# Kernel tuning notes

Measured on AMD Instinct MI355X. Metric: run time of the kernel, lower is better.

Reference implementation:

```python
import jax, jax.numpy as jnp
import numpy as np

B, L, D = 4, 4096, 1024  # batch, seq, d_model == in_features == out_features
E, R = 8, 8              # n_experts, r_base
DH = D // 2              # router hidden


def setup_inputs() -> dict:
    key = jax.random.key(0)
    ks = jax.random.split(key, 8)
    s = 0.02
    return {
        "x": jax.random.normal(ks[0], (B, L, D), dtype=jnp.float32),
        "W_base": jax.random.normal(ks[1], (D, D), dtype=jnp.float32) * s,
        "router_W1": jax.random.normal(ks[2], (DH, D), dtype=jnp.float32) * s,
        "router_b1": jnp.zeros((DH,), dtype=jnp.float32),
        "router_W2": jax.random.normal(ks[3], (E, DH), dtype=jnp.float32) * s,
        "router_b2": jnp.zeros((E,), dtype=jnp.float32),
        "temperature": jnp.asarray(1.0, dtype=jnp.float32),
        "lora_A": jax.random.normal(ks[4], (E, R, D), dtype=jnp.float32) * s,
        "lora_B": jax.random.normal(ks[5], (E, D, R), dtype=jnp.float32) * s,
    }


def reference(x, W_base, router_W1, router_b1, router_W2, router_b2,
              temperature, lora_A, lora_B):
    # Base frozen linear (bias=False): [B,L,D]
    base = jnp.einsum("bld,od->blo", x, W_base)
    # Router (eval mode: dropout inactive). hidden_states = x (Identity projection).
    h = jax.nn.relu(jnp.einsum("bld,hd->blh", x, router_W1) + router_b1)
    logits = (jnp.einsum("blh,eh->ble", h, router_W2) + router_b2) / temperature
    gates = jax.nn.softmax(logits, axis=-1)  # softmax over experts, [B,L,E]
    # All experts' low-rank projections batched: x @ A_e.T -> [B,L,E,R]
    xa = jnp.einsum("bld,erd->bler", x, lora_A)
    # Gate-weighted up-projection and sum over experts: [B,L,D]
    lora_out = jnp.einsum("bler,ble,edr->bld", xa, gates, lora_B)
    return base + lora_out
```

## Files before the change

### kernel.cpp

```cpp
#include <hip/hip_runtime.h>
#include <hip/hip_bf16.h>
#include <stdint.h>
#include <math.h>


#define M_TOK 16384

typedef unsigned short u16;
typedef short bf16x8 __attribute__((ext_vector_type(8)));
typedef float f32x4 __attribute__((ext_vector_type(4)));
typedef __attribute__((address_space(3))) uint32_t lds_u32_t;
typedef __attribute__((address_space(1))) const uint32_t glb_u32_t;

__device__ __forceinline__ u16 f2bf(float f) {
  uint32_t u = __builtin_bit_cast(uint32_t, f);
  return (u16)((u + 0x7fffu + ((u >> 16) & 1u)) >> 16);
}
__device__ __forceinline__ int cvtpk(float lo, float hi) {
  int r;
  asm("v_cvt_pk_bf16_f32 %0, %1, %2" : "=v"(r) : "v"(lo), "v"(hi));
  return r;
}

#define VMCNT(n) asm volatile("s_waitcnt vmcnt(%0)" ::"i"(n) : "memory")
#define LGKM0 asm volatile("s_waitcnt lgkmcnt(0)" ::: "memory")
#define BAR asm volatile("s_barrier" ::: "memory")
#define MEMFENCE asm volatile("" ::: "memory")
#define SP(x) __builtin_amdgcn_s_setprio(x)

__global__ __launch_bounds__(256) void prep_k(const float* __restrict__ Wb,
                                              const float* __restrict__ rW1,
                                              const float* __restrict__ rW2,
                                              const float* __restrict__ loraA,
                                              const float* __restrict__ loraB,
                                              u16* __restrict__ Btb,
                                              u16* __restrict__ W1b,
                                              u16* __restrict__ W2b,
                                              u16* __restrict__ A2b) {
  const int g = blockIdx.x;
  const int tid = threadIdx.x;
  if (g < 1024) {
    int i = g * 256 + tid;
    int idx = i * 4;
    int row = idx >> 10, col = idx & 1023;
    float4 v = ((const float4*)Wb)[i];
    ushort4 o;
    o.x = f2bf(v.x); o.y = f2bf(v.y); o.z = f2bf(v.z); o.w = f2bf(v.w);
    *(ushort4*)(Btb + (size_t)row * 1088 + col) = o;
  } else if (g < 1536) {
    int i = (g - 1024) * 256 + tid;
    float4 v = ((const float4*)rW1)[i];
    ushort4 o;
    o.x = f2bf(v.x); o.y = f2bf(v.y); o.z = f2bf(v.z); o.w = f2bf(v.w);
    ((ushort4*)W1b)[i] = o;
  } else if (g < 1792) {
    int idx = (g - 1536) * 256 + tid;
    int n = idx >> 6, q = idx & 63;
    int e = q >> 3, r = q & 7;
    Btb[(size_t)n * 1088 + 1024 + q] = f2bf(loraB[((size_t)(e * 1024 + n)) * 8 + r]);
  } else if (g < 1856) {
    int i = (g - 1792) * 256 + tid;
    float4 v = ((const float4*)loraA)[i];
    ushort4 o;
    o.x = f2bf(v.x); o.y = f2bf(v.y); o.z = f2bf(v.z); o.w = f2bf(v.w);
    ((ushort4*)A2b)[i] = o;
  } else {
    int i = (g - 1856) * 256 + tid;
    int idx = i * 4;
    int row = idx >> 9, col = idx & 511;
    ushort4 o = {0, 0, 0, 0};
    if (row < 8) {
      float4 v = *(const float4*)(rW2 + (size_t)row * 512 + col);
      o.x = f2bf(v.x); o.y = f2bf(v.y); o.z = f2bf(v.z); o.w = f2bf(v.w);
    }
    ((ushort4*)W2b)[i] = o;
  }
}

__global__ __launch_bounds__(512, 2) void gemm_h(const float* __restrict__ x,
                                                 const u16* __restrict__ W1b,
                                                 const u16* __restrict__ W2bv,
                                                 const u16* __restrict__ A2bv,
                                                 u16* __restrict__ xb,
                                                 u16* __restrict__ wb,
                                                 const float* __restrict__ b1,
                                                 const float* __restrict__ b2,
                                                 const float* __restrict__ temp,
                                                 const int K) {
  constexpr int ABUF = 64 * 128;
  constexpr int BBUF = 512 * 128;
  constexpr int A2BUF = 64 * 128;
  constexpr int BUFB = ABUF + BBUF + A2BUF;
  __shared__ __align__(16) uint8_t lds[2 * BUFB];

  const int tid = threadIdx.x;
  const int lane = tid & 63, w = tid >> 6;
  const int l15 = lane & 15, lhi = lane >> 4;
  const int xorv = (lane & 7) << 4;
  const int c0 = (lhi * 16) ^ xorv;
  const int c1 = (64 + lhi * 16) ^ xorv;

  const int f = blockIdx.x;
  const int m0 = ((f & 7) * 32 + (f >> 3)) * 64;

  const int nk = K >> 6;
  const int rot = (f >> 3) & (nk - 1);
  auto PH = [&](int l) { int lc = l < nk ? l : nk - 1; return (lc + rot) & (nk - 1); };

  const int xrow = tid >> 3, xsub = tid & 7;

  f32x4 acc[4][4] = {};
  f32x4 wacc[4] = {};
  bf16x8 af[4][2], bfv[4][2], a2f[2];
  float4 xA0, xA1, xB0, xB1;

  auto stageBH = [&](int ktp, int b) {
    uint8_t* dst = lds + b * BUFB + ABUF + w * 1024;
#pragma unroll
    for (int i = 0; i < 8; ++i) {
      const int off = i * 8192 + tid * 16;
      const int row = off >> 7;
      const int ss = ((off >> 4) & 7) ^ (row & 7);
      const uint8_t* g =
          (const uint8_t*)W1b + (size_t)row * 2048 + ktp * 128 + ss * 16;
      __builtin_amdgcn_global_load_lds((glb_u32_t*)g, (lds_u32_t*)(dst + i * 8192),
                                       16, 0, 0);
    }
  };
  auto stageA2 = [&](int ktp, int b) {
    uint8_t* dst = lds + b * BUFB + ABUF + BBUF + w * 1024;
    const int off = tid * 16;
    const int row = off >> 7;
    const int ss = ((off >> 4) & 7) ^ (row & 7);
    const uint8_t* g =
        (const uint8_t*)A2bv + (size_t)row * 2048 + ktp * 128 + ss * 16;
    __builtin_amdgcn_global_load_lds((glb_u32_t*)g, (lds_u32_t*)dst, 16, 0, 0);
  };
  auto issueX = [&](int ktp, float4& ra, float4& rb) {
    const float* gp = x + (size_t)(m0 + xrow) * 1024 + ktp * 64 + xsub * 8;
    ra = *(const float4*)gp;
    rb = *(const float4*)(gp + 4);
  };
  auto writeA = [&](int ktp, int b, const float4& ra, const float4& rb) {
    int4 sv;
    sv.x = cvtpk(ra.x, ra.y); sv.y = cvtpk(ra.z, ra.w);
    sv.z = cvtpk(rb.x, rb.y); sv.w = cvtpk(rb.z, rb.w);
    *(int4*)(lds + b * BUFB + xrow * 128 + ((xsub ^ (xrow & 7)) << 4)) = sv;
    *(int4*)(xb + (size_t)(m0 + xrow) * 1024 + ktp * 64 + xsub * 8) = sv;
  };
  auto loadAH = [&](const uint8_t* bufA) {
#pragma unroll
    for (int mf = 0; mf < 4; ++mf) {
      const uint8_t* pr = bufA + (mf * 16 + l15) * 128;
      af[mf][0] = *(const bf16x8*)(pr + c0);
      af[mf][1] = *(const bf16x8*)(pr + c1);
    }
  };
  auto loadBH = [&](const uint8_t* bufB) {
#pragma unroll
    for (int nf = 0; nf < 4; ++nf) {
      const uint8_t* pr = bufB + (w * 64 + nf * 16 + l15) * 128;
      bfv[nf][0] = *(const bf16x8*)(pr + c0);
      bfv[nf][1] = *(const bf16x8*)(pr + c1);
    }
  };
  auto loadA2 = [&](const uint8_t* base) {
    const uint8_t* pr = base + ABUF + BBUF + ((w & 3) * 16 + l15) * 128;
    a2f[0] = *(const bf16x8*)(pr + c0);
    a2f[1] = *(const bf16x8*)(pr + c1);
  };

#define HMM()                                                                  \
  _Pragma("unroll") for (int mf = 0; mf < 4; ++mf)                             \
  _Pragma("unroll") for (int nf = 0; nf < 4; ++nf)                             \
  _Pragma("unroll") for (int ks = 0; ks < 2; ++ks)                             \
      acc[mf][nf] = __builtin_amdgcn_mfma_f32_16x16x32_bf16(                   \
          af[mf][ks], bfv[nf][ks], acc[mf][nf], 0, 0, 0);
#define WMM()                                                                  \
  _Pragma("unroll") for (int mf = 0; mf < 4; ++mf)                             \
  _Pragma("unroll") for (int ks = 0; ks < 2; ++ks)                             \
      wacc[mf] = __builtin_amdgcn_mfma_f32_16x16x32_bf16(                      \
          af[mf][ks], a2f[ks], wacc[mf], 0, 0, 0);

  {
    const float* gp = x + (size_t)(m0 + xrow) * 1024 + rot * 64 + xsub * 8;
    float4 a = *(const float4*)gp, b = *(const float4*)(gp + 4);
    int4 sv;
    sv.x = cvtpk(a.x, a.y); sv.y = cvtpk(a.z, a.w);
    sv.z = cvtpk(b.x, b.y); sv.w = cvtpk(b.z, b.w);
    *(int4*)(lds + xrow * 128 + ((xsub ^ (xrow & 7)) << 4)) = sv;
    *(int4*)(xb + (size_t)(m0 + xrow) * 1024 + rot * 64 + xsub * 8) = sv;
  }
  stageBH(rot, 0);
  stageA2(rot, 0);
  MEMFENCE;
  issueX(PH(1), xA0, xA1);
  VMCNT(2);
  LGKM0;
  BAR;

  const int nit = nk >> 1;
#pragma unroll 1
  for (int it = 0; it < nit; ++it) {
    const int t = it * 2;
    stageBH(PH(t + 1), 1);
    stageA2(PH(t + 1), 1);
    MEMFENCE;
    loadAH(lds);
    loadBH(lds + ABUF);
    loadA2(lds);
    issueX(PH(t + 2), xB0, xB1);
    MEMFENCE;
    VMCNT(11);
    writeA(PH(t + 1), 1, xA0, xA1);
    SP(1); HMM(); WMM(); SP(0);
    LGKM0; VMCNT(3); BAR;
    stageBH(PH(t + 2), 0);
    stageA2(PH(t + 2), 0);
    MEMFENCE;
    loadAH(lds + BUFB);
    loadBH(lds + BUFB + ABUF);
    loadA2(lds + BUFB);
    issueX(PH(t + 3), xA0, xA1);
    MEMFENCE;
    VMCNT(11);
    writeA(PH(t + 2), 0, xB0, xB1);
    SP(1); HMM(); WMM(); SP(0);
    LGKM0; VMCNT(3); BAR;
  }

  u16* hs = (u16*)lds;
  float* g_lds = (float*)(lds + 66560);
  __syncthreads();
#pragma unroll
  for (int mf = 0; mf < 4; ++mf) {
#pragma unroll
    for (int nf = 0; nf < 4; ++nf) {
      const int col = w * 64 + nf * 16 + l15;
#pragma unroll
      for (int j = 0; j < 4; ++j) {
        const int row = mf * 16 + lhi * 4 + j;
        float v = fmaxf(acc[mf][nf][j] + b1[col], 0.f);
        hs[row * 520 + col] = f2bf(v);
      }
    }
  }
  __syncthreads();
  if (w < 4) {
    f32x4 acc2 = {};
#pragma unroll
    for (int ks = 0; ks < 16; ++ks) {
      bf16x8 bfrag = *(const bf16x8*)(W2bv + (size_t)l15 * 512 + ks * 32 + lhi * 8);
      bf16x8 afrag = *(const bf16x8*)(hs + (w * 16 + l15) * 520 + ks * 32 + lhi * 8);
      acc2 = __builtin_amdgcn_mfma_f32_16x16x32_bf16(afrag, bfrag, acc2, 0, 0, 0);
    }
    if (l15 < 8) {
      float t = temp[0];
      float lg[4];
#pragma unroll
      for (int j = 0; j < 4; ++j) lg[j] = (acc2[j] + b2[l15]) / t;
      float mx[4], sm[4];
#pragma unroll
      for (int j = 0; j < 4; ++j) mx[j] = lg[j];
#pragma unroll
      for (int m = 1; m <= 4; m <<= 1)
#pragma unroll
        for (int j = 0; j < 4; ++j) mx[j] = fmaxf(mx[j], __shfl_xor(mx[j], m));
#pragma unroll
      for (int j = 0; j < 4; ++j) { lg[j] = expf(lg[j] - mx[j]); sm[j] = lg[j]; }
#pragma unroll
      for (int m = 1; m <= 4; m <<= 1)
#pragma unroll
        for (int j = 0; j < 4; ++j) sm[j] += __shfl_xor(sm[j], m);
#pragma unroll
      for (int j = 0; j < 4; ++j)
        g_lds[(w * 16 + lhi * 4 + j) * 8 + l15] = lg[j] / sm[j];
    }
  }
  __syncthreads();
  if (w < 4) {
#pragma unroll
    for (int mf = 0; mf < 4; ++mf) {
#pragma unroll
      for (int j = 0; j < 4; ++j) {
        const int row = mf * 16 + lhi * 4 + j;
        const int col = w * 16 + l15;
        float v = wacc[mf][j] * g_lds[row * 8 + (col >> 3)];
        wb[(size_t)(m0 + row) * 64 + col] = f2bf(v);
      }
    }
  }
}

#define MFMA_Q2(mh, nh, AF, BF)                                                \
  _Pragma("unroll") for (int im2 = 0; im2 < 4; ++im2)                          \
  _Pragma("unroll") for (int in2 = 0; in2 < 2; ++in2)                          \
  _Pragma("unroll") for (int ks = 0; ks < 2; ++ks)                             \
      acc[(mh) * 4 + im2][(nh) * 2 + in2] =                                    \
          __builtin_amdgcn_mfma_f32_16x16x32_bf16(                             \
              AF[im2][ks], BF[in2][ks],                                        \
              acc[(mh) * 4 + im2][(nh) * 2 + in2], 0, 0, 0);

__global__ __launch_bounds__(512, 2) void gemm_out(const u16* __restrict__ A,
                                                   const u16* __restrict__ Bt,
                                                   const u16* __restrict__ A2,
                                                   float* __restrict__ C,
                                                   const int N, const int K,
                                                   const int lda, const int ldb) {
  constexpr int BM = 256, BN = 256;
  constexpr int VMC = 4;
  constexpr int BUFB = (BM + BN) * 128;

  __shared__ __align__(16) uint8_t lds[2 * BUFB];

  const int tid = threadIdx.x;
  const int lane = tid & 63, w = tid >> 6;
  const int wr = w >> 2, wcn = w & 3;
  const int l15 = lane & 15, lhi = lane >> 4;
  const int xorv = (lane & 7) << 4;
  const int c0 = (lhi * 16) ^ xorv;
  const int c1 = (64 + lhi * 16) ^ xorv;

  const int f = blockIdx.x;
  const int idx = (f & 7) * 32 + (f >> 3);
  const int gx = N / BN;
  const int m0 = (idx / gx) * BM;
  const int n0 = (idx % gx) * BN;

  const size_t lda_b = (size_t)lda * 2, ldb_b = (size_t)ldb * 2;
  const int nk = K >> 6;
  const int arow0 = (wr * (BM / 2) + l15) * 128;
  const int brow0 = (wcn * (BN / 4) + l15) * 128;

  f32x4 acc[8][4] = {};
  bf16x8 A0f[4][2], A1f[4][2];
  bf16x8 B0f[2][2], B1f[2][2];

  auto stageA = [&](int h, int kt, int b) {
    const int ktc = kt < nk ? kt : nk - 1;
    const bool last = (ktc == nk - 1);
    uint8_t* dst = lds + b * BUFB + h * (BM * 64) + w * 1024;
#pragma unroll
    for (int i = 0; i < 2; ++i) {
      const int off = i * 8192 + tid * 16;
      const int row = h * (BM / 2) + (off >> 7);
      const int ss = ((off >> 4) & 7) ^ (row & 7);
      const uint8_t* g =
          last ? (const uint8_t*)A2 + (size_t)(m0 + row) * 128 + ss * 16
               : (const uint8_t*)A + (size_t)(m0 + row) * lda_b + ktc * 128 + ss * 16;
      __builtin_amdgcn_global_load_lds((glb_u32_t*)g, (lds_u32_t*)(dst + i * 8192),
                                       16, 0, 0);
    }
  };
  auto stageB = [&](int h, int kt, int b) {
    const int ktc = kt < nk ? kt : nk - 1;
    uint8_t* dst = lds + b * BUFB + BM * 128 + h * (BN * 64) + w * 1024;
#pragma unroll
    for (int i = 0; i < 2; ++i) {
      const int off = i * 8192 + tid * 16;
      const int row = h * (BN / 2) + (off >> 7);
      const int ss = ((off >> 4) & 7) ^ (row & 7);
      const uint8_t* g =
          (const uint8_t*)Bt + (size_t)(n0 + row) * ldb_b + ktc * 128 + ss * 16;
      __builtin_amdgcn_global_load_lds((glb_u32_t*)g, (lds_u32_t*)(dst + i * 8192),
                                       16, 0, 0);
    }
  };
  auto loadA = [&](int mh, const uint8_t* buf, bf16x8 (&dst)[4][2]) {
#pragma unroll
    for (int im2 = 0; im2 < 4; ++im2) {
      const uint8_t* p = buf + arow0 + mh * (4 * 2048) + im2 * 2048;
      dst[im2][0] = *(const bf16x8*)(p + c0);
      dst[im2][1] = *(const bf16x8*)(p + c1);
    }
  };
  auto loadB = [&](int nh, const uint8_t* buf, bf16x8 (&dst)[2][2]) {
#pragma unroll
    for (int in2 = 0; in2 < 2; ++in2) {
      const uint8_t* p = buf + BM * 128 + brow0 + nh * (2 * 2048) + in2 * 2048;
      dst[in2][0] = *(const bf16x8*)(p + c0);
      dst[in2][1] = *(const bf16x8*)(p + c1);
    }
  };

  const uint8_t* b0 = lds;
  const uint8_t* b1 = lds + BUFB;

  stageA(0, 0, 0); stageA(1, 0, 0);
  stageB(0, 0, 0); stageB(1, 0, 0);
  stageB(0, 1, 1); stageB(1, 1, 1);
  VMCNT(VMC); BAR;
  loadA(0, b0, A0f); loadB(0, b0, B0f);

  const int NIT = nk >> 1;
#pragma unroll 1
  for (int it = 0; it < NIT; ++it) {
    const int t = it * 2;
    stageA(0, t + 1, 1);
    BAR;
    SP(1); MFMA_Q2(0, 0, A0f, B0f); SP(0);
    loadB(1, b0, B1f);
    BAR;
    stageA(1, t + 1, 1);
    BAR;
    SP(1); MFMA_Q2(0, 1, A0f, B1f); SP(0);
    loadA(1, b0, A1f);
    BAR;
    stageB(0, t + 2, 0);
    BAR;
    SP(1); MFMA_Q2(1, 1, A1f, B1f); SP(0);
    BAR;
    stageB(1, t + 2, 0);
    VMCNT(VMC);
    BAR;
    SP(1); MFMA_Q2(1, 0, A1f, B0f); SP(0);
    loadA(0, b1, A0f); loadB(0, b1, B0f);
    BAR;
    stageA(0, t + 2, 0);
    BAR;
    SP(1); MFMA_Q2(0, 0, A0f, B0f); SP(0);
    loadB(1, b1, B1f);
    BAR;
    stageA(1, t + 2, 0);
    BAR;
    SP(1); MFMA_Q2(0, 1, A0f, B1f); SP(0);
    loadA(1, b1, A1f);
    BAR;
    stageB(0, t + 3, 1);
    BAR;
    SP(1); MFMA_Q2(1, 1, A1f, B1f); SP(0);
    BAR;
    stageB(1, t + 3, 1);
    VMCNT(VMC);
    BAR;
    SP(1); MFMA_Q2(1, 0, A1f, B0f); SP(0);
    loadA(0, b0, A0f); loadB(0, b0, B0f);
    BAR;
  }

  if (nk & 1) {
    SP(1); MFMA_Q2(0, 0, A0f, B0f); SP(0);
    loadB(1, b0, B1f);
    SP(1); MFMA_Q2(0, 1, A0f, B1f); SP(0);
    loadA(1, b0, A1f);
    SP(1); MFMA_Q2(1, 1, A1f, B1f); MFMA_Q2(1, 0, A1f, B0f); SP(0);
  }

#pragma unroll
  for (int im = 0; im < 8; ++im) {
#pragma unroll
    for (int in_ = 0; in_ < 4; ++in_) {
      const int col = n0 + wcn * 64 + in_ * 16 + l15;
#pragma unroll
      for (int j = 0; j < 4; ++j) {
        const int row = m0 + wr * 128 + im * 16 + lhi * 4 + j;
        C[(size_t)row * N + col] = acc[im][in_][j];
      }
    }
  }
}

extern "C" void kernel_launch(void* const* d_in, const int* in_sizes, int n_in,
                              void* d_out, int out_size, void* d_ws, size_t ws_size,
                              hipStream_t stream) {
  const float* x     = (const float*)d_in[0];
  const float* Wb    = (const float*)d_in[1];
  const float* rW1   = (const float*)d_in[2];
  const float* rb1   = (const float*)d_in[3];
  const float* rW2   = (const float*)d_in[4];
  const float* rb2   = (const float*)d_in[5];
  const float* temp  = (const float*)d_in[6];
  const float* loraA = (const float*)d_in[7];
  const float* loraB = (const float*)d_in[8];
  float* out = (float*)d_out;

  uint8_t* p = (uint8_t*)d_ws;
  u16* xb    = (u16*)p;   p += (size_t)M_TOK * 1024 * 2;
  u16* wb    = (u16*)p;   p += (size_t)M_TOK * 64 * 2;
  u16* Btb   = (u16*)p;   p += (size_t)1024 * 1088 * 2;
  u16* W1b   = (u16*)p;   p += (size_t)512 * 1024 * 2;
  u16* W2b   = (u16*)p;   p += (size_t)16 * 512 * 2;
  u16* A2b   = (u16*)p;   p += (size_t)64 * 1024 * 2;

  prep_k<<<1864, 256, 0, stream>>>(Wb, rW1, rW2, loraA, loraB, Btb, W1b, W2b, A2b);

  gemm_h<<<256, 512, 0, stream>>>(x, W1b, W2b, A2b, xb, wb, rb1, rb2, temp, 1024);

  gemm_out<<<256, 512, 0, stream>>>(xb, Btb, wb, out, 1024, 1088, 1024, 1088);
}
```

Measured before the change: 80.74 us.

## Move x bf16 conversion into prep kernel and stream A tile via direct LDS loads

The fp32-to-bf16 conversion of x moves out of the router GEMM and into the prep kernel, which now writes xb for all tokens. gemm_h then loads its A tile from xb with global_load_lds like the weight tiles, and the hand-unrolled two-stage loop becomes a simpler single-step double-buffered loop. This takes register staging and conversion work off the GEMM's critical path. In exchange it adds a separate pass that reads 64MB of x and writes 32MB of xb, then reads xb back in gemm_h.

```diff
diff --git a/kernel.cpp b/kernel.cpp
--- a/kernel.cpp
+++ b/kernel.cpp
@@ -16,56 +16,58 @@
   uint32_t u = __builtin_bit_cast(uint32_t, f);
   return (u16)((u + 0x7fffu + ((u >> 16) & 1u)) >> 16);
 }
-__device__ __forceinline__ int cvtpk(float lo, float hi) {
-  int r;
-  asm("v_cvt_pk_bf16_f32 %0, %1, %2" : "=v"(r) : "v"(lo), "v"(hi));
-  return r;
-}
 
 #define VMCNT(n) asm volatile("s_waitcnt vmcnt(%0)" ::"i"(n) : "memory")
 #define LGKM0 asm volatile("s_waitcnt lgkmcnt(0)" ::: "memory")
 #define BAR asm volatile("s_barrier" ::: "memory")
-#define MEMFENCE asm volatile("" ::: "memory")
 #define SP(x) __builtin_amdgcn_s_setprio(x)
 
-__global__ __launch_bounds__(256) void prep_k(const float* __restrict__ Wb,
+__global__ __launch_bounds__(256) void prep_k(const float* __restrict__ x,
+                                              const float* __restrict__ Wb,
                                               const float* __restrict__ rW1,
                                               const float* __restrict__ rW2,
                                               const float* __restrict__ loraA,
                                               const float* __restrict__ loraB,
+                                              u16* __restrict__ xb,
                                               u16* __restrict__ Btb,
                                               u16* __restrict__ W1b,
                                               u16* __restrict__ W2b,
                                               u16* __restrict__ A2b) {
   const int g = blockIdx.x;
   const int tid = threadIdx.x;
-  if (g < 1024) {
+  if (g < 16384) {
     int i = g * 256 + tid;
+    float4 v = ((const float4*)x)[i];
+    ushort4 o;
+    o.x = f2bf(v.x); o.y = f2bf(v.y); o.z = f2bf(v.z); o.w = f2bf(v.w);
+    ((ushort4*)xb)[i] = o;
+  } else if (g < 17408) {
+    int i = (g - 16384) * 256 + tid;
     int idx = i * 4;
     int row = idx >> 10, col = idx & 1023;
     float4 v = ((const float4*)Wb)[i];
     ushort4 o;
     o.x = f2bf(v.x); o.y = f2bf(v.y); o.z = f2bf(v.z); o.w = f2bf(v.w);
     *(ushort4*)(Btb + (size_t)row * 1088 + col) = o;
-  } else if (g < 1536) {
-    int i = (g - 1024) * 256 + tid;
+  } else if (g < 17920) {
+    int i = (g - 17408) * 256 + tid;
     float4 v = ((const float4*)rW1)[i];
     ushort4 o;
     o.x = f2bf(v.x); o.y = f2bf(v.y); o.z = f2bf(v.z); o.w = f2bf(v.w);
     ((ushort4*)W1b)[i] = o;
-  } else if (g < 1792) {
-    int idx = (g - 1536) * 256 + tid;
+  } else if (g < 18176) {
+    int idx = (g - 17920) * 256 + tid;
     int n = idx >> 6, q = idx & 63;
     int e = q >> 3, r = q & 7;
     Btb[(size_t)n * 1088 + 1024 + q] = f2bf(loraB[((size_t)(e * 1024 + n)) * 8 + r]);
-  } else if (g < 1856) {
-    int i = (g - 1792) * 256 + tid;
+  } else if (g < 18240) {
+    int i = (g - 18176) * 256 + tid;
     float4 v = ((const float4*)loraA)[i];
     ushort4 o;
     o.x = f2bf(v.x); o.y = f2bf(v.y); o.z = f2bf(v.z); o.w = f2bf(v.w);
     ((ushort4*)A2b)[i] = o;
   } else {
-    int i = (g - 1856) * 256 + tid;
+    int i = (g - 18240) * 256 + tid;
     int idx = i * 4;
     int row = idx >> 9, col = idx & 511;
     ushort4 o = {0, 0, 0, 0};
@@ -77,11 +79,10 @@
   }
 }
 
-__global__ __launch_bounds__(512, 2) void gemm_h(const float* __restrict__ x,
+__global__ __launch_bounds__(512, 2) void gemm_h(const u16* __restrict__ xb,
                                                  const u16* __restrict__ W1b,
                                                  const u16* __restrict__ W2bv,
                                                  const u16* __restrict__ A2bv,
-                                                 u16* __restrict__ xb,
                                                  u16* __restrict__ wb,
                                                  const float* __restrict__ b1,
                                                  const float* __restrict__ b2,
@@ -107,13 +108,19 @@
   const int rot = (f >> 3) & (nk - 1);
   auto PH = [&](int l) { int lc = l < nk ? l : nk - 1; return (lc + rot) & (nk - 1); };
 
-  const int xrow = tid >> 3, xsub = tid & 7;
-
   f32x4 acc[4][4] = {};
   f32x4 wacc[4] = {};
   bf16x8 af[4][2], bfv[4][2], a2f[2];
-  float4 xA0, xA1, xB0, xB1;
-
+
+  auto stageA = [&](int ktp, int b) {
+    uint8_t* dst = lds + b * BUFB + w * 1024;
+    const int off = tid * 16;
+    const int row = off >> 7;
+    const int ss = ((off >> 4) & 7) ^ (row & 7);
+    const uint8_t* g =
+        (const uint8_t*)xb + (size_t)(m0 + row) * 2048 + ktp * 128 + ss * 16;
+    __builtin_amdgcn_global_load_lds((glb_u32_t*)g, (lds_u32_t*)dst, 16, 0, 0);
+  };
   auto stageBH = [&](int ktp, int b) {
     uint8_t* dst = lds + b * BUFB + ABUF + w * 1024;
 #pragma unroll
@@ -135,18 +142,6 @@
     const uint8_t* g =
         (const uint8_t*)A2bv + (size_t)row * 2048 + ktp * 128 + ss * 16;
     __builtin_amdgcn_global_load_lds((glb_u32_t*)g, (lds_u32_t*)dst, 16, 0, 0);
-  };
-  auto issueX = [&](int ktp, float4& ra, float4& rb) {
-    const float* gp = x + (size_t)(m0 + xrow) * 1024 + ktp * 64 + xsub * 8;
-    ra = *(const float4*)gp;
-    rb = *(const float4*)(gp + 4);
-  };
-  auto writeA = [&](int ktp, int b, const float4& ra, const float4& rb) {
-    int4 sv;
-    sv.x = cvtpk(ra.x, ra.y); sv.y = cvtpk(ra.z, ra.w);
-    sv.z = cvtpk(rb.x, rb.y); sv.w = cvtpk(rb.z, rb.w);
-    *(int4*)(lds + b * BUFB + xrow * 128 + ((xsub ^ (xrow & 7)) << 4)) = sv;
-    *(int4*)(xb + (size_t)(m0 + xrow) * 1024 + ktp * 64 + xsub * 8) = sv;
   };
   auto loadAH = [&](const uint8_t* bufA) {
 #pragma unroll
@@ -182,51 +177,25 @@
       wacc[mf] = __builtin_amdgcn_mfma_f32_16x16x32_bf16(                      \
           af[mf][ks], a2f[ks], wacc[mf], 0, 0, 0);
 
-  {
-    const float* gp = x + (size_t)(m0 + xrow) * 1024 + rot * 64 + xsub * 8;
-    float4 a = *(const float4*)gp, b = *(const float4*)(gp + 4);
-    int4 sv;
-    sv.x = cvtpk(a.x, a.y); sv.y = cvtpk(a.z, a.w);
-    sv.z = cvtpk(b.x, b.y); sv.w = cvtpk(b.z, b.w);
-    *(int4*)(lds + xrow * 128 + ((xsub ^ (xrow & 7)) << 4)) = sv;
-    *(int4*)(xb + (size_t)(m0 + xrow) * 1024 + rot * 64 + xsub * 8) = sv;
-  }
+  stageA(rot, 0);
   stageBH(rot, 0);
   stageA2(rot, 0);
-  MEMFENCE;
-  issueX(PH(1), xA0, xA1);
-  VMCNT(2);
-  LGKM0;
-  BAR;
-
-  const int nit = nk >> 1;
+
 #pragma unroll 1
-  for (int it = 0; it < nit; ++it) {
-    const int t = it * 2;
-    stageBH(PH(t + 1), 1);
-    stageA2(PH(t + 1), 1);
-    MEMFENCE;
-    loadAH(lds);
-    loadBH(lds + ABUF);
-    loadA2(lds);
-    issueX(PH(t + 2), xB0, xB1);
-    MEMFENCE;
-    VMCNT(11);
-    writeA(PH(t + 1), 1, xA0, xA1);
+  for (int t = 0; t < nk; ++t) {
+    const int p = t & 1, q = p ^ 1;
+    const uint8_t* bp = (const uint8_t*)lds + p * BUFB;
+    stageA(PH(t + 1), q);
+    stageBH(PH(t + 1), q);
+    stageA2(PH(t + 1), q);
+    VMCNT(10);
+    BAR;
+    loadAH(bp);
+    loadBH(bp + ABUF);
+    loadA2(bp);
     SP(1); HMM(); WMM(); SP(0);
-    LGKM0; VMCNT(3); BAR;
-    stageBH(PH(t + 2), 0);
-    stageA2(PH(t + 2), 0);
-    MEMFENCE;
-    loadAH(lds + BUFB);
-    loadBH(lds + BUFB + ABUF);
-    loadA2(lds + BUFB);
-    issueX(PH(t + 3), xA0, xA1);
-    MEMFENCE;
-    VMCNT(11);
-    writeA(PH(t + 2), 0, xB0, xB1);
-    SP(1); HMM(); WMM(); SP(0);
-    LGKM0; VMCNT(3); BAR;
+    LGKM0;
+    BAR;
   }
 
   u16* hs = (u16*)lds;
@@ -482,9 +451,10 @@
   u16* W2b   = (u16*)p;   p += (size_t)16 * 512 * 2;
   u16* A2b   = (u16*)p;   p += (size_t)64 * 1024 * 2;
 
-  prep_k<<<1864, 256, 0, stream>>>(Wb, rW1, rW2, loraA, loraB, Btb, W1b, W2b, A2b);
-
-  gemm_h<<<256, 512, 0, stream>>>(x, W1b, W2b, A2b, xb, wb, rb1, rb2, temp, 1024);
+  prep_k<<<18248, 256, 0, stream>>>(x, Wb, rW1, rW2, loraA, loraB,
+                                    xb, Btb, W1b, W2b, A2b);
+
+  gemm_h<<<256, 512, 0, stream>>>(xb, W1b, W2b, A2b, wb, rb1, rb2, temp, 1024);
 
   gemm_out<<<256, 512, 0, stream>>>(xb, Btb, wb, out, 1024, 1088, 1024, 1088);
 }
```

Result: slower. 90.14 us (+11.6%).
